# Optimization experiments

Hardware: AMD Instinct MI355X
Metric: run time of the kernel (lower is better)

Reference implementation:

```python
import jax, jax.numpy as jnp
import numpy as np

BT, L, F, N = 8, 8192, 128, 16


def setup_inputs() -> dict:
    key = jax.random.key(0)
    ks = jax.random.split(key, 7)
    scale = 1.0 / np.sqrt(F)
    x = jax.random.normal(ks[0], (BT, L, F), dtype=jnp.float32)
    Wb = jax.random.normal(ks[1], (F, N), dtype=jnp.float32) * scale
    bb = jax.random.normal(ks[2], (N,), dtype=jnp.float32) * 0.01
    Wc = jax.random.normal(ks[3], (F, N), dtype=jnp.float32) * scale
    bc = jax.random.normal(ks[4], (N,), dtype=jnp.float32) * 0.01
    Wd = jax.random.normal(ks[5], (F, 1), dtype=jnp.float32) * scale
    bd = jax.random.normal(ks[6], (1,), dtype=jnp.float32) * 0.01
    # diagonal HiPPO-like spectrum (A is diagonal in the source: torch.diag(eigenvalues))
    A = -(jnp.arange(N, dtype=jnp.float32) + 1.0)
    return {"x": x, "Wb": Wb, "bb": bb, "Wc": Wc, "bc": bc, "Wd": Wd, "bd": bd, "A": A}


def reference(x, Wb, bb, Wc, bc, Wd, bd, A):
    # input-dependent SSM parameters (S6 / selective scan)
    B = x @ Wb + bb                      # [BT, L, N]
    C = x @ Wc + bc                      # [BT, L, N]
    delta = jax.nn.softplus(x @ Wd + bd)  # [BT, L, 1]
    # ZOH discretization with diagonal A
    dA = jnp.exp(delta * A)              # [BT, L, N]
    dB = (dA - 1.0) / A * B              # [BT, L, N]

    def step(h, inp):
        dA_t, dB_t, x_t, C_t = inp       # [BT,N],[BT,N],[BT,F],[BT,N]
        # h: [BT, F, N]; each feature channel has its own N-dim state
        h = dA_t[:, None, :] * h + dB_t[:, None, :] * x_t[:, :, None]
        y = jnp.einsum('bfn,bn->bf', h, C_t)
        return h, y

    h0 = jnp.zeros((x.shape[0], x.shape[2], A.shape[0]), dtype=x.dtype)
    xs = (jnp.swapaxes(dA, 0, 1), jnp.swapaxes(dB, 0, 1),
          jnp.swapaxes(x, 0, 1), jnp.swapaxes(C, 0, 1))
    _, ys = jax.lax.scan(step, h0, xs)   # ys: [L, BT, F]
    return jnp.swapaxes(ys, 0, 1)        # [BT, L, F]
```

## Files before the change

kernel.cpp:

```cpp
#include <hip/hip_runtime.h>


#define BTc   8
#define Lseq  8192
#define Fdim  128
#define Ndim  16
#define CH    128
#define LC    64

__global__ __launch_bounds__(64) void k_fused(
    const float* __restrict__ x,
    const float* __restrict__ Wb, const float* __restrict__ bb,
    const float* __restrict__ Wc, const float* __restrict__ bc,
    const float* __restrict__ Wd, const float* __restrict__ bd,
    const float* __restrict__ A,
    float* __restrict__ ylocal,
    float* __restrict__ q, float* __restrict__ E, float* __restrict__ S)
{
    __shared__ float Gl[LC][52];
    const int lane = threadIdx.x;
    const int c = blockIdx.x, b = blockIdx.y;
    const size_t tok0 = (size_t)b * Lseq + (size_t)c * LC;

    const float4* xt = reinterpret_cast<const float4*>(x + (tok0 + lane) * Fdim);
    float acc[33];
#pragma unroll
    for (int j = 0; j < 33; ++j) acc[j] = 0.f;

#pragma unroll 4
    for (int kk = 0; kk < 32; ++kk) {
        float4 xv = xt[kk];
        const float* wb0 = Wb + kk * 64;
        const float* wc0 = Wc + kk * 64;
        const float* wd0 = Wd + kk * 4;
#pragma unroll
        for (int j = 0; j < 16; ++j) {
            acc[j]      = fmaf(xv.x, wb0[j],      acc[j]);
            acc[j]      = fmaf(xv.y, wb0[16 + j], acc[j]);
            acc[j]      = fmaf(xv.z, wb0[32 + j], acc[j]);
            acc[j]      = fmaf(xv.w, wb0[48 + j], acc[j]);
            acc[16 + j] = fmaf(xv.x, wc0[j],      acc[16 + j]);
            acc[16 + j] = fmaf(xv.y, wc0[16 + j], acc[16 + j]);
            acc[16 + j] = fmaf(xv.z, wc0[32 + j], acc[16 + j]);
            acc[16 + j] = fmaf(xv.w, wc0[48 + j], acc[16 + j]);
        }
        acc[32] = fmaf(xv.x, wd0[0], acc[32]);
        acc[32] = fmaf(xv.y, wd0[1], acc[32]);
        acc[32] = fmaf(xv.z, wd0[2], acc[32]);
        acc[32] = fmaf(xv.w, wd0[3], acc[32]);
    }

    float v = acc[32] + bd[0];
    float delta = fmaxf(v, 0.f) + log1pf(expf(-fabsf(v)));
    float cum = delta;
#pragma unroll
    for (int off = 1; off < 64; off <<= 1) {
        float up = __shfl_up(cum, off);
        cum += (lane >= off) ? up : 0.f;
    }
    if (lane == LC - 1) S[b * CH + c] = cum;

    {
        float dAv[16], dBv[16], Cv[16], Ev[16];
#pragma unroll
        for (int n = 0; n < 16; ++n) {
            float An = A[n];
            float dA = expf(delta * An);
            dAv[n] = dA;
            dBv[n] = (dA - 1.f) / An * (acc[n] + bb[n]);
            Cv[n]  = acc[16 + n] + bc[n];
            Ev[n]  = Cv[n] * expf(An * cum);
        }
        float4* gr = reinterpret_cast<float4*>(&Gl[lane][0]);
#pragma unroll
        for (int p = 0; p < 4; ++p) {
            gr[p]     = make_float4(dAv[4*p], dAv[4*p+1], dAv[4*p+2], dAv[4*p+3]);
            gr[4 + p] = make_float4(dBv[4*p], dBv[4*p+1], dBv[4*p+2], dBv[4*p+3]);
            gr[8 + p] = make_float4(Cv[4*p],  Cv[4*p+1],  Cv[4*p+2],  Cv[4*p+3]);
        }
        float4* Ep = reinterpret_cast<float4*>(E + ((size_t)(b * CH + c) * LC + lane) * 16);
#pragma unroll
        for (int p = 0; p < 4; ++p)
            Ep[p] = make_float4(Ev[4*p], Ev[4*p+1], Ev[4*p+2], Ev[4*p+3]);
    }

    float h0[16], h1[16];
#pragma unroll
    for (int n = 0; n < 16; ++n) { h0[n] = 0.f; h1[n] = 0.f; }

    const float* xs = x + tok0 * Fdim;
    float* yp = ylocal + tok0 * Fdim;
#pragma unroll 2
    for (int t = 0; t < LC; ++t) {
        float xv0 = xs[t * Fdim + lane];
        float xv1 = xs[t * Fdim + lane + 64];
        const float4* gp = reinterpret_cast<const float4*>(&Gl[t][0]);
        float da[16], db[16], cc[16];
#pragma unroll
        for (int p = 0; p < 4; ++p) {
            float4 a4 = gp[p], b4 = gp[4 + p], c4 = gp[8 + p];
            da[4*p] = a4.x; da[4*p+1] = a4.y; da[4*p+2] = a4.z; da[4*p+3] = a4.w;
            db[4*p] = b4.x; db[4*p+1] = b4.y; db[4*p+2] = b4.z; db[4*p+3] = b4.w;
            cc[4*p] = c4.x; cc[4*p+1] = c4.y; cc[4*p+2] = c4.z; cc[4*p+3] = c4.w;
        }
        float y0 = 0.f, y1 = 0.f;
#pragma unroll
        for (int n = 0; n < 16; ++n) {
            h0[n] = fmaf(da[n], h0[n], db[n] * xv0);
            h1[n] = fmaf(da[n], h1[n], db[n] * xv1);
            y0 = fmaf(cc[n], h0[n], y0);
            y1 = fmaf(cc[n], h1[n], y1);
        }
        yp[t * Fdim + lane]      = y0;
        yp[t * Fdim + lane + 64] = y1;
    }

    float4* qp0 = reinterpret_cast<float4*>(q + ((size_t)(b * CH + c) * Fdim + lane) * 16);
    float4* qp1 = reinterpret_cast<float4*>(q + ((size_t)(b * CH + c) * Fdim + lane + 64) * 16);
#pragma unroll
    for (int p = 0; p < 4; ++p) {
        qp0[p] = make_float4(h0[4*p], h0[4*p+1], h0[4*p+2], h0[4*p+3]);
        qp1[p] = make_float4(h1[4*p], h1[4*p+1], h1[4*p+2], h1[4*p+3]);
    }
}

__global__ __launch_bounds__(256) void k_chunkscan(
    const float* __restrict__ q, const float* __restrict__ S,
    const float* __restrict__ A, float* __restrict__ Hin)
{
    int id = blockIdx.x * 256 + threadIdx.x;
    int b  = id >> 11;
    int fn = id & 2047;
    int n  = id & 15;
    float An = A[n];
    float H = 0.f;
    size_t qb = (size_t)b * CH * 2048 + fn;
    const float* Sb = S + b * CH;
    for (int cg = 0; cg < CH; cg += 16) {
        float Sr[16], qr[16];
#pragma unroll
        for (int i = 0; i < 16; ++i) {
            Sr[i] = Sb[cg + i];
            qr[i] = q[qb + (size_t)(cg + i) * 2048];
        }
#pragma unroll
        for (int i = 0; i < 16; ++i) {
            Hin[qb + (size_t)(cg + i) * 2048] = H;
            H = fmaf(__expf(An * Sr[i]), H, qr[i]);
        }
    }
}

__global__ __launch_bounds__(128) void k_correct(
    const float* __restrict__ Hin, const float* __restrict__ E,
    float* __restrict__ y)
{
    __shared__ float El[LC][16];
    const int c = blockIdx.x, b = blockIdx.y;
    const int f = threadIdx.x;

    const float4* Eg = reinterpret_cast<const float4*>(E + (size_t)(b * CH + c) * LC * 16);
    float4* Es = reinterpret_cast<float4*>(&El[0][0]);
    for (int i = f; i < LC * 4; i += 128) Es[i] = Eg[i];

    float hv[16];
    const float4* hp = reinterpret_cast<const float4*>(Hin + ((size_t)(b * CH + c) * Fdim + f) * 16);
#pragma unroll
    for (int p = 0; p < 4; ++p) {
        float4 t4 = hp[p];
        hv[4*p] = t4.x; hv[4*p+1] = t4.y; hv[4*p+2] = t4.z; hv[4*p+3] = t4.w;
    }
    __syncthreads();

    float* yp = y + ((size_t)b * Lseq + (size_t)c * LC) * Fdim + f;
#pragma unroll 4
    for (int t = 0; t < LC; ++t) {
        const float4* ep = reinterpret_cast<const float4*>(&El[t][0]);
        float acc = 0.f;
#pragma unroll
        for (int p = 0; p < 4; ++p) {
            float4 e4 = ep[p];
            acc = fmaf(e4.x, hv[4*p],     acc);
            acc = fmaf(e4.y, hv[4*p + 1], acc);
            acc = fmaf(e4.z, hv[4*p + 2], acc);
            acc = fmaf(e4.w, hv[4*p + 3], acc);
        }
        yp[t * Fdim] += acc;
    }
}

extern "C" void kernel_launch(void* const* d_in, const int* in_sizes, int n_in,
                              void* d_out, int out_size, void* d_ws, size_t ws_size,
                              hipStream_t stream) {
    const float* x  = (const float*)d_in[0];
    const float* Wb = (const float*)d_in[1];
    const float* bb = (const float*)d_in[2];
    const float* Wc = (const float*)d_in[3];
    const float* bc = (const float*)d_in[4];
    const float* Wd = (const float*)d_in[5];
    const float* bd = (const float*)d_in[6];
    const float* A  = (const float*)d_in[7];
    float* y = (float*)d_out;

    float* q   = (float*)d_ws;
    float* Hin = q   + (size_t)BTc * CH * Fdim * Ndim;
    float* E   = Hin + (size_t)BTc * CH * Fdim * Ndim;
    float* S   = E   + (size_t)BTc * CH * LC * Ndim;

    k_fused<<<dim3(CH, BTc), 64, 0, stream>>>(x, Wb, bb, Wc, bc, Wd, bd, A,
                                              y, q, E, S);
    k_chunkscan<<<dim3(BTc * Fdim * Ndim / 256), 256, 0, stream>>>(q, S, A, Hin);
    k_correct<<<dim3(CH, BTc), 128, 0, stream>>>(Hin, E, y);
}
```

Before: 91.37 us.

## Split fused projection/scan kernel into split-K projection and per-feature scan kernels

The fused kernel is split into two. k_pre runs the x-projections with 256 threads using a 4-way split over K, reduces the partial sums through shared memory, and writes dA/dB/C per token to a new global buffer G. k_scan then runs the chunk-local recurrence with 128 threads, one feature per thread, instead of 64 threads each handling two features. The aim is more parallelism and occupancy than the 64-thread fused block allowed, at the cost of an extra launch and a global round trip for G (48 floats per token).

```diff
diff --git a/kernel.cpp b/kernel.cpp
--- a/kernel.cpp
+++ b/kernel.cpp
@@ -8,120 +8,134 @@
 #define CH    128
 #define LC    64
 
-__global__ __launch_bounds__(64) void k_fused(
+__global__ __launch_bounds__(256) void k_pre(
     const float* __restrict__ x,
     const float* __restrict__ Wb, const float* __restrict__ bb,
     const float* __restrict__ Wc, const float* __restrict__ bc,
     const float* __restrict__ Wd, const float* __restrict__ bd,
-    const float* __restrict__ A,
-    float* __restrict__ ylocal,
-    float* __restrict__ q, float* __restrict__ E, float* __restrict__ S)
-{
-    __shared__ float Gl[LC][52];
-    const int lane = threadIdx.x;
+    const float* __restrict__ A,  float* __restrict__ G,
+    float* __restrict__ E, float* __restrict__ S)
+{
+    __shared__ float Pl[33][4][66];
+    const int tid = threadIdx.x;
+    const int ks = tid >> 6, lane = tid & 63;
     const int c = blockIdx.x, b = blockIdx.y;
     const size_t tok0 = (size_t)b * Lseq + (size_t)c * LC;
 
-    const float4* xt = reinterpret_cast<const float4*>(x + (tok0 + lane) * Fdim);
+    const float4* xt = reinterpret_cast<const float4*>(x + (tok0 + lane) * Fdim + ks * 32);
     float acc[33];
 #pragma unroll
     for (int j = 0; j < 33; ++j) acc[j] = 0.f;
 
-#pragma unroll 4
-    for (int kk = 0; kk < 32; ++kk) {
+#pragma unroll 2
+    for (int kk = 0; kk < 8; ++kk) {
         float4 xv = xt[kk];
-        const float* wb0 = Wb + kk * 64;
-        const float* wc0 = Wc + kk * 64;
-        const float* wd0 = Wd + kk * 4;
+        const float* wbp = Wb + (ks * 32 + kk * 4) * 16;
+        const float* wcp = Wc + (ks * 32 + kk * 4) * 16;
+        const float* wdp = Wd + (ks * 32 + kk * 4);
 #pragma unroll
         for (int j = 0; j < 16; ++j) {
-            acc[j]      = fmaf(xv.x, wb0[j],      acc[j]);
-            acc[j]      = fmaf(xv.y, wb0[16 + j], acc[j]);
-            acc[j]      = fmaf(xv.z, wb0[32 + j], acc[j]);
-            acc[j]      = fmaf(xv.w, wb0[48 + j], acc[j]);
-            acc[16 + j] = fmaf(xv.x, wc0[j],      acc[16 + j]);
-            acc[16 + j] = fmaf(xv.y, wc0[16 + j], acc[16 + j]);
-            acc[16 + j] = fmaf(xv.z, wc0[32 + j], acc[16 + j]);
-            acc[16 + j] = fmaf(xv.w, wc0[48 + j], acc[16 + j]);
-        }
-        acc[32] = fmaf(xv.x, wd0[0], acc[32]);
-        acc[32] = fmaf(xv.y, wd0[1], acc[32]);
-        acc[32] = fmaf(xv.z, wd0[2], acc[32]);
-        acc[32] = fmaf(xv.w, wd0[3], acc[32]);
-    }
-
-    float v = acc[32] + bd[0];
-    float delta = fmaxf(v, 0.f) + log1pf(expf(-fabsf(v)));
-    float cum = delta;
-#pragma unroll
-    for (int off = 1; off < 64; off <<= 1) {
-        float up = __shfl_up(cum, off);
-        cum += (lane >= off) ? up : 0.f;
-    }
-    if (lane == LC - 1) S[b * CH + c] = cum;
-
-    {
-        float dAv[16], dBv[16], Cv[16], Ev[16];
+            acc[j] = fmaf(xv.x, wbp[j],      acc[j]);
+            acc[j] = fmaf(xv.y, wbp[16 + j], acc[j]);
+            acc[j] = fmaf(xv.z, wbp[32 + j], acc[j]);
+            acc[j] = fmaf(xv.w, wbp[48 + j], acc[j]);
+            acc[16 + j] = fmaf(xv.x, wcp[j],      acc[16 + j]);
+            acc[16 + j] = fmaf(xv.y, wcp[16 + j], acc[16 + j]);
+            acc[16 + j] = fmaf(xv.z, wcp[32 + j], acc[16 + j]);
+            acc[16 + j] = fmaf(xv.w, wcp[48 + j], acc[16 + j]);
+        }
+        acc[32] = fmaf(xv.x, wdp[0], acc[32]);
+        acc[32] = fmaf(xv.y, wdp[1], acc[32]);
+        acc[32] = fmaf(xv.z, wdp[2], acc[32]);
+        acc[32] = fmaf(xv.w, wdp[3], acc[32]);
+    }
+#pragma unroll
+    for (int j = 0; j < 33; ++j) Pl[j][ks][lane] = acc[j];
+    __syncthreads();
+
+    if (tid < 64) {
+        float s[33];
+#pragma unroll
+        for (int j = 0; j < 33; ++j)
+            s[j] = (Pl[j][0][lane] + Pl[j][1][lane]) + (Pl[j][2][lane] + Pl[j][3][lane]);
+
+        float v = s[32] + bd[0];
+        float delta = fmaxf(v, 0.f) + log1pf(expf(-fabsf(v)));
+        float cum = delta;
+#pragma unroll
+        for (int off = 1; off < 64; off <<= 1) {
+            float up = __shfl_up(cum, off);
+            cum += (lane >= off) ? up : 0.f;
+        }
+        if (lane == LC - 1) S[b * CH + c] = cum;
+
+        float out[48], Ev[16];
 #pragma unroll
         for (int n = 0; n < 16; ++n) {
             float An = A[n];
             float dA = expf(delta * An);
-            dAv[n] = dA;
-            dBv[n] = (dA - 1.f) / An * (acc[n] + bb[n]);
-            Cv[n]  = acc[16 + n] + bc[n];
-            Ev[n]  = Cv[n] * expf(An * cum);
-        }
-        float4* gr = reinterpret_cast<float4*>(&Gl[lane][0]);
-#pragma unroll
-        for (int p = 0; p < 4; ++p) {
-            gr[p]     = make_float4(dAv[4*p], dAv[4*p+1], dAv[4*p+2], dAv[4*p+3]);
-            gr[4 + p] = make_float4(dBv[4*p], dBv[4*p+1], dBv[4*p+2], dBv[4*p+3]);
-            gr[8 + p] = make_float4(Cv[4*p],  Cv[4*p+1],  Cv[4*p+2],  Cv[4*p+3]);
-        }
+            float Cn = s[16 + n] + bc[n];
+            out[n]      = dA;
+            out[16 + n] = (dA - 1.f) / An * (s[n] + bb[n]);
+            out[32 + n] = Cn;
+            Ev[n] = Cn * expf(An * cum);
+        }
+        float4* Gr = reinterpret_cast<float4*>(G + (tok0 + lane) * 48);
+#pragma unroll
+        for (int p = 0; p < 12; ++p)
+            Gr[p] = make_float4(out[4*p], out[4*p+1], out[4*p+2], out[4*p+3]);
         float4* Ep = reinterpret_cast<float4*>(E + ((size_t)(b * CH + c) * LC + lane) * 16);
 #pragma unroll
         for (int p = 0; p < 4; ++p)
             Ep[p] = make_float4(Ev[4*p], Ev[4*p+1], Ev[4*p+2], Ev[4*p+3]);
     }
-
-    float h0[16], h1[16];
-#pragma unroll
-    for (int n = 0; n < 16; ++n) { h0[n] = 0.f; h1[n] = 0.f; }
-
-    const float* xs = x + tok0 * Fdim;
-    float* yp = ylocal + tok0 * Fdim;
+}
+
+__global__ __launch_bounds__(128, 2) void k_scan(
+    const float* __restrict__ x, const float* __restrict__ G,
+    float* __restrict__ y, float* __restrict__ q)
+{
+    __shared__ float Gl[LC][48];
+    const int c = blockIdx.x, b = blockIdx.y;
+    const int f = threadIdx.x;
+    const size_t tok0 = (size_t)b * Lseq + (size_t)c * LC;
+
+    const float4* Gg = reinterpret_cast<const float4*>(G + tok0 * 48);
+    float4* Gs = reinterpret_cast<float4*>(&Gl[0][0]);
+    for (int idx = f; idx < LC * 12; idx += 128) Gs[idx] = Gg[idx];
+    __syncthreads();
+
+    float h[16];
+#pragma unroll
+    for (int n = 0; n < 16; ++n) h[n] = 0.f;
+
+    const float* xp = x + tok0 * Fdim + f;
+    float*       yp = y + tok0 * Fdim + f;
 #pragma unroll 2
     for (int t = 0; t < LC; ++t) {
-        float xv0 = xs[t * Fdim + lane];
-        float xv1 = xs[t * Fdim + lane + 64];
-        const float4* gp = reinterpret_cast<const float4*>(&Gl[t][0]);
+        float xv = xp[t * Fdim];
+        const float4* gp4 = reinterpret_cast<const float4*>(&Gl[t][0]);
         float da[16], db[16], cc[16];
 #pragma unroll
         for (int p = 0; p < 4; ++p) {
-            float4 a4 = gp[p], b4 = gp[4 + p], c4 = gp[8 + p];
-            da[4*p] = a4.x; da[4*p+1] = a4.y; da[4*p+2] = a4.z; da[4*p+3] = a4.w;
-            db[4*p] = b4.x; db[4*p+1] = b4.y; db[4*p+2] = b4.z; db[4*p+3] = b4.w;
-            cc[4*p] = c4.x; cc[4*p+1] = c4.y; cc[4*p+2] = c4.z; cc[4*p+3] = c4.w;
-        }
-        float y0 = 0.f, y1 = 0.f;
+            float4 va = gp4[p], vb = gp4[4 + p], vc = gp4[8 + p];
+            da[4*p] = va.x; da[4*p+1] = va.y; da[4*p+2] = va.z; da[4*p+3] = va.w;
+            db[4*p] = vb.x; db[4*p+1] = vb.y; db[4*p+2] = vb.z; db[4*p+3] = vb.w;
+            cc[4*p] = vc.x; cc[4*p+1] = vc.y; cc[4*p+2] = vc.z; cc[4*p+3] = vc.w;
+        }
+        float yacc = 0.f;
 #pragma unroll
         for (int n = 0; n < 16; ++n) {
-            h0[n] = fmaf(da[n], h0[n], db[n] * xv0);
-            h1[n] = fmaf(da[n], h1[n], db[n] * xv1);
-            y0 = fmaf(cc[n], h0[n], y0);
-            y1 = fmaf(cc[n], h1[n], y1);
-        }
-        yp[t * Fdim + lane]      = y0;
-        yp[t * Fdim + lane + 64] = y1;
-    }
-
-    float4* qp0 = reinterpret_cast<float4*>(q + ((size_t)(b * CH + c) * Fdim + lane) * 16);
-    float4* qp1 = reinterpret_cast<float4*>(q + ((size_t)(b * CH + c) * Fdim + lane + 64) * 16);
-#pragma unroll
-    for (int p = 0; p < 4; ++p) {
-        qp0[p] = make_float4(h0[4*p], h0[4*p+1], h0[4*p+2], h0[4*p+3]);
-        qp1[p] = make_float4(h1[4*p], h1[4*p+1], h1[4*p+2], h1[4*p+3]);
-    }
+            h[n] = fmaf(da[n], h[n], db[n] * xv);
+            yacc = fmaf(cc[n], h[n], yacc);
+        }
+        yp[t * Fdim] = yacc;
+    }
+
+    float4* qp = reinterpret_cast<float4*>(q + ((size_t)(b * CH + c) * Fdim + f) * 16);
+#pragma unroll
+    for (int p = 0; p < 4; ++p)
+        qp[p] = make_float4(h[4*p], h[4*p+1], h[4*p+2], h[4*p+3]);
 }
 
 __global__ __launch_bounds__(256) void k_chunkscan(
@@ -151,7 +165,7 @@
     }
 }
 
-__global__ __launch_bounds__(128) void k_correct(
+__global__ __launch_bounds__(128, 2) void k_correct(
     const float* __restrict__ Hin, const float* __restrict__ E,
     float* __restrict__ y)
 {
@@ -202,13 +216,14 @@
     const float* A  = (const float*)d_in[7];
     float* y = (float*)d_out;
 
-    float* q   = (float*)d_ws;
+    float* G   = (float*)d_ws;
+    float* q   = G   + (size_t)BTc * Lseq * 48;
     float* Hin = q   + (size_t)BTc * CH * Fdim * Ndim;
     float* E   = Hin + (size_t)BTc * CH * Fdim * Ndim;
-    float* S   = E   + (size_t)BTc * CH * LC * Ndim;
-
-    k_fused<<<dim3(CH, BTc), 64, 0, stream>>>(x, Wb, bb, Wc, bc, Wd, bd, A,
-                                              y, q, E, S);
+    float* S   = E   + (size_t)BTc * Lseq * Ndim;
+
+    k_pre<<<dim3(CH, BTc), 256, 0, stream>>>(x, Wb, bb, Wc, bc, Wd, bd, A, G, E, S);
+    k_scan<<<dim3(CH, BTc), 128, 0, stream>>>(x, G, y, q);
     k_chunkscan<<<dim3(BTc * Fdim * Ndim / 256), 256, 0, stream>>>(q, S, A, Hin);
     k_correct<<<dim3(CH, BTc), 128, 0, stream>>>(Hin, E, y);
 }
```

Measured after the change: 102.3 us. 1.12x slower.
